# Kernel tuning notes

Hardware: AMD Instinct MI355X
Metric: run time of the kernel (lower is better)

Reference implementation:

```python
import jax, jax.numpy as jnp
import numpy as np

N, L, D = 2, 2048, 96
H, DK, DV = 4, 16, 16
OUT = 96
SPATIAL = H * (3 + 1 + 3)  # points + distance + direction per head
INF = 100000.0
EPS_DIR = 1e-10
EPS_LN = 1e-5


def setup_inputs() -> dict:
    key = jax.random.key(0)
    ks = jax.random.split(key, 10)
    return {
        "x": jax.random.normal(ks[0], (N, L, D), jnp.float32),
        "pos_CA": jax.random.normal(ks[1], (N, L, 3), jnp.float32),
        "pos_CB": jax.random.normal(ks[2], (N, L, 3), jnp.float32),
        "frame": jax.random.normal(ks[3], (N, L, 3, 3), jnp.float32),
        "mask": jnp.ones((N, L), dtype=bool),
        "Wq": jax.random.normal(ks[4], (D, H * DK), jnp.float32) * 0.1,
        "Wk": jax.random.normal(ks[5], (D, H * DK), jnp.float32) * 0.1,
        "Wv": jax.random.normal(ks[6], (D, H * DV), jnp.float32) * 0.1,
        "Wo": jax.random.normal(ks[7], (H * DV + SPATIAL, OUT), jnp.float32) * 0.1,
        "bo": jnp.zeros((OUT,), jnp.float32),
        "gamma": jnp.ones((OUT,), jnp.float32),
        "beta": jnp.zeros((OUT,), jnp.float32),
    }


def reference(x, pos_CA, pos_CB, frame, mask, Wq, Wk, Wv, Wo, bo, gamma, beta):
    n, l, _ = x.shape
    q = (x @ Wq).reshape(n, l, H, DK)
    k = (x @ Wk).reshape(n, l, H, DK)
    v = (x @ Wv).reshape(n, l, H, DV)

    # logits (N, L_q, L_k, H)
    logits = jnp.einsum('blhd,bkhd->blkh', q, k)
    mask_row = mask[:, :, None, None]           # (N, L, 1, 1)
    mask_pair = mask_row & mask[:, None, :, None]
    logits = jnp.where(mask_pair, logits, logits - INF)
    alpha = jax.nn.softmax(logits, axis=2)
    alpha = jnp.where(mask_row, alpha, 0.0)

    feat_node = jnp.einsum('blkh,bkhd->blhd', alpha, v).reshape(n, l, H * DV)

    # rel_pos[b,l,k] = CB[k] - CA[l]
    rel_pos = pos_CB[:, None, :, :] - pos_CA[:, :, None, :]
    atom_pos_bias = jnp.einsum('blkh,blkd->blhd', alpha, rel_pos)  # (N,L,H,3)
    feat_distance = jnp.linalg.norm(atom_pos_bias, axis=-1, keepdims=True)
    feat_points = jnp.einsum('blij,blhj->blhi', frame, atom_pos_bias)
    feat_direction = feat_points / (jnp.linalg.norm(feat_points, axis=-1, keepdims=True) + EPS_DIR)

    feat_spatial = jnp.concatenate([
        feat_points.reshape(n, l, H * 3),
        feat_distance.reshape(n, l, H),
        feat_direction.reshape(n, l, H * 3),
    ], axis=-1)

    feat_all = jnp.concatenate([feat_node, feat_spatial], axis=-1) @ Wo + bo
    feat_all = jnp.where(mask[:, :, None], feat_all, 0.0)

    # output_dim == input_dim -> residual + LayerNorm
    h = x + feat_all
    mu = jnp.mean(h, axis=-1, keepdims=True)
    var = jnp.var(h, axis=-1, keepdims=True)
    return (h - mu) / jnp.sqrt(var + EPS_LN) * gamma + beta
```

## Files before the change

### kernel.cpp

```cpp
#include <hip/hip_runtime.h>
#include <hip/hip_fp16.h>

typedef _Float16 f16;
typedef _Float16 v4h __attribute__((ext_vector_type(4)));
typedef _Float16 v8h __attribute__((ext_vector_type(8)));
typedef short    v4s __attribute__((ext_vector_type(4)));
typedef short    v8s __attribute__((ext_vector_type(8)));
typedef float    v4f __attribute__((ext_vector_type(4)));

#define NB   2
#define LSEQ 2048
#define DIM  96
#define NH   4
#define ROWS 4096
#define NT16 128
#define NT32 64
#define OUTD 96
#define SHIFT 12.0f
#define LOG2E   1.4426950408889634f
#define NSH2    (-17.312340490667562f)

#if __has_builtin(__builtin_amdgcn_mfma_f32_16x16x16f16)
#define MFMA16_F16(A, B, C) __builtin_amdgcn_mfma_f32_16x16x16f16((A), (B), (C), 0, 0, 0)
#else
static __device__ __forceinline__ v4f mfma16_f16_asm(v4h a, v4h b, v4f c) {
    asm volatile("v_mfma_f32_16x16x16_f16 %0, %1, %2, %0"
                 : "+v"(c) : "v"(a), "v"(b));
    return c;
}
#define MFMA16_F16(A, B, C) mfma16_f16_asm((A), (B), (C))
#endif
#define MFMA32_F16(A, B, C) __builtin_amdgcn_mfma_f32_16x16x32_f16((A), (B), (C), 0, 0, 0)
#define MFMA_BF16(A, B, C)  __builtin_amdgcn_mfma_f32_16x16x32_bf16((A), (B), (C), 0, 0, 0)

#if __has_builtin(__builtin_amdgcn_exp2f)
#define EXP2F(x) __builtin_amdgcn_exp2f(x)
#else
#define EXP2F(x) exp2f(x)
#endif

static __device__ __forceinline__ short f2bf(float f) {
    unsigned u = __builtin_bit_cast(unsigned, f);
    u += 0x7FFF + ((u >> 16) & 1);
    return (short)(u >> 16);
}

__global__ __launch_bounds__(256) void proj_kernel(
    const float* __restrict__ x,
    const float* __restrict__ posCB,
    const float* __restrict__ Wq,
    const float* __restrict__ Wk,
    const float* __restrict__ Wv,
    f16*   __restrict__ qf,
    f16*   __restrict__ kf2,
    short* __restrict__ vf,
    short* __restrict__ pf)
{
    const int tid  = threadIdx.x;
    const int wv   = tid >> 6;
    const int lane = tid & 63;
    const int quad = lane >> 4, c16 = lane & 15;
    const int bid  = blockIdx.x;
    const int b    = bid >> 7, t16 = bid & 127;
    const int row0 = bid * 16;

    __shared__ v8h wfragv[12 * 3 * 65];
    f16* wf = (f16*)wfragv;

    v8h xb[3];
    #pragma unroll
    for (int kt = 0; kt < 3; ++kt) {
        const float* xp = x + (size_t)(row0 + c16) * DIM + kt * 32 + quad * 8;
        const v4f x0 = *(const v4f*)xp;
        const v4f x1 = *(const v4f*)(xp + 4);
        v8h h;
        #pragma unroll
        for (int j = 0; j < 4; ++j) { h[j] = (f16)x0[j]; h[4 + j] = (f16)x1[j]; }
        xb[kt] = h;
    }

    {
        const float* Ws[3] = {Wq, Wk, Wv};
        #pragma unroll
        for (int widx = 0; widx < 3; ++widx) {
            const float* W = Ws[widx];
            #pragma unroll
            for (int it = 0; it < 24; ++it) {
                const int flat = it * 256 + tid;
                const int dd = flat >> 6, n = flat & 63;
                const int frag = (widx * 4 + (n >> 4)) * 3 + (dd >> 5);
                wf[frag * 520 + (((dd >> 3) & 3) * 16 + (n & 15)) * 8 + (dd & 7)]
                    = (f16)W[flat];
            }
        }
    }
    __syncthreads();

    #pragma unroll
    for (int u = 0; u < 3; ++u) {
        const int dt = wv * 3 + u;
        v4f acc = {0.f, 0.f, 0.f, 0.f};
        #pragma unroll
        for (int kt = 0; kt < 3; ++kt)
            acc = MFMA32_F16(wfragv[(dt * 3 + kt) * 65 + lane], xb[kt], acc);

        const int widx = dt >> 2, sub = dt & 3;
        const int bh = b * NH + sub;
        if (widx == 0) {
            v4h o;
            #pragma unroll
            for (int r = 0; r < 4; ++r) o[r] = (f16)acc[r];
            *(v4h*)(qf + ((size_t)(bh * NT16 + t16)) * 256 + (c16 + 16 * quad) * 4) = o;
        } else if (widx == 1) {
            v4h o;
            #pragma unroll
            for (int r = 0; r < 4; ++r) o[r] = (f16)acc[r];
            *(v4h*)(kf2 + ((size_t)(bh * NT32 + (t16 >> 1))) * 512
                        + lane * 8 + (t16 & 1) * 4) = o;
        } else {
            short* dst = vf + ((size_t)(bh * NT32 + (t16 >> 1))) * 512
                            + (t16 & 1) * 4 + (c16 & 3);
            #pragma unroll
            for (int r = 0; r < 4; ++r)
                dst[(quad * 4 + r + 16 * (c16 >> 2)) * 8] = f2bf(acc[r]);
        }
    }

    if (bid < NB * NT32) {
        const int b2 = bid >> 6, t2 = bid & 63;
        const int lf = tid & 63, jh = tid >> 6;
        const int n = lf & 15, qS = lf >> 4;
        #pragma unroll
        for (int u2 = 0; u2 < 2; ++u2) {
            const int jSp = jh * 2 + u2;
            const int key = t2 * 32 + (jSp < 4 ? qS * 4 + jSp : 16 + qS * 4 + (jSp & 3));
            float val = 0.f;
            if (n < 3)       val = posCB[((size_t)(b2 * LSEQ + key)) * 3 + n];
            else if (n == 3) val = 1.f;
            pf[((size_t)(b2 * NT32 + t2)) * 512 + lf * 8 + jSp] = f2bf(val);
        }
    }
}

__global__ __launch_bounds__(1024, 1) void attn_epi_kernel(
    const f16*   __restrict__ qf,
    const f16*   __restrict__ kf2,
    const short* __restrict__ vf,
    const short* __restrict__ pf,
    const float* __restrict__ x,
    const float* __restrict__ posCA,
    const float* __restrict__ frame,
    const float* __restrict__ Wo,
    const float* __restrict__ bo,
    const float* __restrict__ gamma,
    const float* __restrict__ beta,
    float*       __restrict__ out)
{
    const int w     = threadIdx.x >> 6;
    const int lane  = threadIdx.x & 63;
    const int head  = w & 3, kq = w >> 2;
    const int b     = blockIdx.x >> 7;
    const int qt    = blockIdx.x & 127;
    const int bh    = b * NH + head;
    const int quad  = lane >> 4, c16 = lane & 15;

    __shared__ float comb[16][64][12];
    __shared__ float feat[16][100];
    __shared__ float aps[16][NH][3];

    const v4h aq = *(const v4h*)(qf + ((size_t)(bh * NT16 + qt)) * 256 + lane * 4);
    const f16*   kb = kf2 + (size_t)bh * NT32 * 512;
    const short* vb = vf  + (size_t)bh * NT32 * 512;
    const short* pb = pf  + (size_t)b  * NT32 * 512;

    v4f O  = {0.f, 0.f, 0.f, 0.f};
    v4f Wa = {0.f, 0.f, 0.f, 0.f};
    const v4f zero = {0.f, 0.f, 0.f, 0.f};
    float psum = 0.f;

    const int t0 = kq * 16;
    v8h bk = *(const v8h*)(kb + (size_t)t0 * 512 + lane * 8);
    v8s bv = *(const v8s*)(vb + (size_t)t0 * 512 + lane * 8);
    v8s bp = *(const v8s*)(pb + (size_t)t0 * 512 + lane * 8);

#define ATTN_STEP(BK, BV, BP) do {                                          \
        const v4h bk0 = __builtin_shufflevector((BK), (BK), 0, 1, 2, 3);    \
        const v4h bk1 = __builtin_shufflevector((BK), (BK), 4, 5, 6, 7);    \
        const v4f S0 = MFMA16_F16(bk0, aq, zero);                           \
        const v4f S1 = MFMA16_F16(bk1, aq, zero);                           \
        v8s ap;                                                             \
        _Pragma("unroll")                                                   \
        for (int r = 0; r < 4; ++r) {                                       \
            const float e0 = EXP2F(fmaf(S0[r], LOG2E, NSH2));               \
            const float e1 = EXP2F(fmaf(S1[r], LOG2E, NSH2));               \
            ap[r]     = f2bf(e0);                                           \
            ap[4 + r] = f2bf(e1);                                           \
            psum += e0 + e1;                                                \
        }                                                                   \
        O  = MFMA_BF16(ap, (BV), O);                                        \
        Wa = MFMA_BF16(ap, (BP), Wa);                                       \
    } while (0)

    #pragma unroll 3
    for (int i = 0; i < 15; ++i) {
        const v8h bkc = bk; const v8s bvc = bv, bpc = bp;
        const size_t off = (size_t)(t0 + i + 1) * 512 + lane * 8;
        bk = *(const v8h*)(kb + off);
        bv = *(const v8s*)(vb + off);
        bp = *(const v8s*)(pb + off);
        ATTN_STEP(bkc, bvc, bpc);
    }
    ATTN_STEP(bk, bv, bp);
#undef ATTN_STEP

    {
        float* cb = &comb[w][lane][0];
        *(v4f*)cb       = O;
        *(v4f*)(cb + 4) = Wa;
        cb[8] = psum;
    }
    __syncthreads();

    const int rowg0 = b * LSEQ + qt * 16;

    if (w < 4) {
        #pragma unroll
        for (int k2 = 1; k2 < 4; ++k2) {
            const float* cb = &comb[k2 * 4 + w][lane][0];
            O    += *(const v4f*)cb;
            Wa   += *(const v4f*)(cb + 4);
            psum += cb[8];
        }
        psum += __shfl_xor(psum, 16);
        psum += __shfl_xor(psum, 32);
        const float inv = 1.f / psum;
        #pragma unroll
        for (int r = 0; r < 4; ++r) {
            const float ir = __shfl(inv, quad * 4 + r);
            feat[quad * 4 + r][w * 16 + c16] = O[r] * ir;
            if (c16 < 3)
                aps[quad * 4 + r][w][c16] = Wa[r] * ir;
        }
    }
    __syncthreads();

    if (lane < 4) {
        const int hh = lane;
        const int grow = rowg0 + w;
        float apb[3];
        #pragma unroll
        for (int j = 0; j < 3; ++j)
            apb[j] = aps[w][hh][j] - posCA[(size_t)grow * 3 + j];
        const float dist = sqrtf(apb[0]*apb[0] + apb[1]*apb[1] + apb[2]*apb[2]);
        float fp[3];
        #pragma unroll
        for (int i = 0; i < 3; ++i) {
            float a = 0.f;
            #pragma unroll
            for (int j = 0; j < 3; ++j)
                a = fmaf(frame[(size_t)grow * 9 + i * 3 + j], apb[j], a);
            fp[i] = a;
        }
        const float fpn  = sqrtf(fp[0]*fp[0] + fp[1]*fp[1] + fp[2]*fp[2]);
        const float rinv = 1.f / (fpn + 1e-10f);
        #pragma unroll
        for (int i = 0; i < 3; ++i) {
            feat[w][64 + hh * 3 + i] = fp[i];
            feat[w][80 + hh * 3 + i] = fp[i] * rinv;
        }
        feat[w][76 + hh] = dist;
    }
    __syncthreads();

    {
        const int grow = rowg0 + w;

        float acc0 = bo[lane];
        #pragma unroll 8
        for (int r2 = 0; r2 < 92; ++r2)
            acc0 = fmaf(feat[w][r2], Wo[r2 * OUTD + lane], acc0);
        const float hv0 = acc0 + x[(size_t)grow * DIM + lane];

        float hv1 = 0.f;
        if (lane < 32) {
            float acc1 = bo[64 + lane];
            #pragma unroll 8
            for (int r2 = 0; r2 < 92; ++r2)
                acc1 = fmaf(feat[w][r2], Wo[r2 * OUTD + 64 + lane], acc1);
            hv1 = acc1 + x[(size_t)grow * DIM + 64 + lane];
        }

        float ls = hv0 + hv1;
        float lq = fmaf(hv0, hv0, hv1 * hv1);
        #pragma unroll
        for (int off = 32; off > 0; off >>= 1) {
            ls += __shfl_xor(ls, off);
            lq += __shfl_xor(lq, off);
        }
        const float mu  = ls * (1.f / OUTD);
        const float var = lq * (1.f / OUTD) - mu * mu;
        const float rs  = rsqrtf(var + 1e-5f);

        out[(size_t)grow * OUTD + lane] = (hv0 - mu) * rs * gamma[lane] + beta[lane];
        if (lane < 32)
            out[(size_t)grow * OUTD + 64 + lane] =
                (hv1 - mu) * rs * gamma[64 + lane] + beta[64 + lane];
    }
}

extern "C" void kernel_launch(void* const* d_in, const int* in_sizes, int n_in,
                              void* d_out, int out_size, void* d_ws, size_t ws_size,
                              hipStream_t stream)
{
    const float* x     = (const float*)d_in[0];
    const float* posCA = (const float*)d_in[1];
    const float* posCB = (const float*)d_in[2];
    const float* frame = (const float*)d_in[3];
    const float* Wq    = (const float*)d_in[5];
    const float* Wk    = (const float*)d_in[6];
    const float* Wv    = (const float*)d_in[7];
    const float* Wo    = (const float*)d_in[8];
    const float* bo    = (const float*)d_in[9];
    const float* gamma = (const float*)d_in[10];
    const float* beta  = (const float*)d_in[11];

    f16*   qf  = (f16*)d_ws;
    f16*   kf2 = qf + (size_t)8 * NT16 * 256;
    short* vf  = (short*)(kf2 + (size_t)8 * NT32 * 512);
    short* pf  = vf + (size_t)8 * NT32 * 512;

    proj_kernel<<<256, 256, 0, stream>>>(x, posCB, Wq, Wk, Wv, qf, kf2, vf, pf);
    attn_epi_kernel<<<NB * NT16, 1024, 0, stream>>>(qf, kf2, vf, pf,
                                                    x, posCA, frame,
                                                    Wo, bo, gamma, beta,
                                                    (float*)d_out);
}
```

Baseline: 104.8 us.

## Split attention and epilogue kernels; each block handles one head over 64 queries

Moves the attention into its own kernel. Each block now serves one head and four 16-query tiles, so every K/V/P fragment loaded is reused across four query tiles instead of one. Key tiles are split across all 16 waves, and partial sums are reduced through shared memory per query tile. The attention result and the point bias go to a workspace buffer that a separate epilogue kernel reads to do the spatial features, the Wo projection and LayerNorm. This adds a third launch, a global round-trip through the workspace, and four sync-heavy reduction rounds per block.

Result: slower. 113.8 us (+8.6%).

```diff
diff --git a/kernel.cpp b/kernel.cpp
--- a/kernel.cpp
+++ b/kernel.cpp
@@ -4,7 +4,6 @@
 typedef _Float16 f16;
 typedef _Float16 v4h __attribute__((ext_vector_type(4)));
 typedef _Float16 v8h __attribute__((ext_vector_type(8)));
-typedef short    v4s __attribute__((ext_vector_type(4)));
 typedef short    v8s __attribute__((ext_vector_type(8)));
 typedef float    v4f __attribute__((ext_vector_type(4)));
 
@@ -142,11 +141,107 @@
     }
 }
 
-__global__ __launch_bounds__(1024, 1) void attn_epi_kernel(
+__global__ __launch_bounds__(1024, 1) void attn_kernel(
     const f16*   __restrict__ qf,
     const f16*   __restrict__ kf2,
     const short* __restrict__ vf,
     const short* __restrict__ pf,
+    float*       __restrict__ med)
+{
+    const int tid  = threadIdx.x;
+    const int w    = tid >> 6;
+    const int lane = tid & 63;
+    const int bid  = blockIdx.x;
+    const int b    = bid >> 7, rem = bid & 127;
+    const int qg   = rem >> 2, head = rem & 3;
+    const int bh   = b * NH + head;
+
+    __shared__ float comb[16][64][12];
+    __shared__ float invl[16];
+
+    const f16*   kb = kf2 + (size_t)bh * NT32 * 512;
+    const short* vb = vf  + (size_t)bh * NT32 * 512;
+    const short* pb = pf  + (size_t)b  * NT32 * 512;
+
+    v4h aq[4];
+    #pragma unroll
+    for (int g = 0; g < 4; ++g)
+        aq[g] = *(const v4h*)(qf + ((size_t)(bh * NT16 + qg * 4 + g)) * 256 + lane * 4);
+
+    const v4f zero = {0.f, 0.f, 0.f, 0.f};
+    v4f O[4], Wa[4];
+    float psum[4] = {0.f, 0.f, 0.f, 0.f};
+    #pragma unroll
+    for (int g = 0; g < 4; ++g) { O[g] = zero; Wa[g] = zero; }
+
+    const int t0 = w * 4;
+    v8h bk = *(const v8h*)(kb + (size_t)t0 * 512 + lane * 8);
+    v8s bv = *(const v8s*)(vb + (size_t)t0 * 512 + lane * 8);
+    v8s bp = *(const v8s*)(pb + (size_t)t0 * 512 + lane * 8);
+
+    #pragma unroll
+    for (int i = 0; i < 4; ++i) {
+        const v8h bkc = bk; const v8s bvc = bv, bpc = bp;
+        if (i < 3) {
+            const size_t off = (size_t)(t0 + i + 1) * 512 + lane * 8;
+            bk = *(const v8h*)(kb + off);
+            bv = *(const v8s*)(vb + off);
+            bp = *(const v8s*)(pb + off);
+        }
+        const v4h bk0 = __builtin_shufflevector(bkc, bkc, 0, 1, 2, 3);
+        const v4h bk1 = __builtin_shufflevector(bkc, bkc, 4, 5, 6, 7);
+        #pragma unroll
+        for (int g = 0; g < 4; ++g) {
+            const v4f S0 = MFMA16_F16(bk0, aq[g], zero);
+            const v4f S1 = MFMA16_F16(bk1, aq[g], zero);
+            v8s ap;
+            #pragma unroll
+            for (int r = 0; r < 4; ++r) {
+                const float e0 = EXP2F(fmaf(S0[r], LOG2E, NSH2));
+                const float e1 = EXP2F(fmaf(S1[r], LOG2E, NSH2));
+                ap[r]     = f2bf(e0);
+                ap[4 + r] = f2bf(e1);
+                psum[g] += e0 + e1;
+            }
+            O[g]  = MFMA_BF16(ap, bvc, O[g]);
+            Wa[g] = MFMA_BF16(ap, bpc, Wa[g]);
+        }
+    }
+
+    const int rowbase = b * LSEQ + qg * 64;
+    for (int g = 0; g < 4; ++g) {
+        float* cb = &comb[w][lane][0];
+        *(v4f*)cb       = O[g];
+        *(v4f*)(cb + 4) = Wa[g];
+        cb[8] = psum[g];
+        __syncthreads();
+
+        float s = 0.f;
+        if (w < 9) {
+            #pragma unroll
+            for (int w2 = 0; w2 < 16; ++w2)
+                s += comb[w2][lane][w];
+            if (w == 8) {
+                s += __shfl_xor(s, 16);
+                s += __shfl_xor(s, 32);
+                if (lane < 16) invl[lane] = 1.f / s;
+            }
+        }
+        __syncthreads();
+
+        if (w < 8) {
+            const int qrow = (lane >> 4) * 4 + (w & 3);
+            const int cc   = lane & 15;
+            const float val = s * invl[qrow];
+            const size_t grow = (size_t)(rowbase + g * 16 + qrow);
+            if (w < 4)        med[grow * 80 + head * 16 + cc] = val;
+            else if (cc < 3)  med[grow * 80 + 64 + head * 3 + cc] = val;
+        }
+    }
+}
+
+__global__ __launch_bounds__(1024) void epi_kernel(
+    const float* __restrict__ med,
     const float* __restrict__ x,
     const float* __restrict__ posCA,
     const float* __restrict__ frame,
@@ -156,101 +251,21 @@
     const float* __restrict__ beta,
     float*       __restrict__ out)
 {
-    const int w     = threadIdx.x >> 6;
-    const int lane  = threadIdx.x & 63;
-    const int head  = w & 3, kq = w >> 2;
-    const int b     = blockIdx.x >> 7;
-    const int qt    = blockIdx.x & 127;
-    const int bh    = b * NH + head;
-    const int quad  = lane >> 4, c16 = lane & 15;
-
-    __shared__ float comb[16][64][12];
+    const int w    = threadIdx.x >> 6;
+    const int lane = threadIdx.x & 63;
+    const int grow = blockIdx.x * 16 + w;
+
     __shared__ float feat[16][100];
-    __shared__ float aps[16][NH][3];
-
-    const v4h aq = *(const v4h*)(qf + ((size_t)(bh * NT16 + qt)) * 256 + lane * 4);
-    const f16*   kb = kf2 + (size_t)bh * NT32 * 512;
-    const short* vb = vf  + (size_t)bh * NT32 * 512;
-    const short* pb = pf  + (size_t)b  * NT32 * 512;
-
-    v4f O  = {0.f, 0.f, 0.f, 0.f};
-    v4f Wa = {0.f, 0.f, 0.f, 0.f};
-    const v4f zero = {0.f, 0.f, 0.f, 0.f};
-    float psum = 0.f;
-
-    const int t0 = kq * 16;
-    v8h bk = *(const v8h*)(kb + (size_t)t0 * 512 + lane * 8);
-    v8s bv = *(const v8s*)(vb + (size_t)t0 * 512 + lane * 8);
-    v8s bp = *(const v8s*)(pb + (size_t)t0 * 512 + lane * 8);
-
-#define ATTN_STEP(BK, BV, BP) do {                                          \
-        const v4h bk0 = __builtin_shufflevector((BK), (BK), 0, 1, 2, 3);    \
-        const v4h bk1 = __builtin_shufflevector((BK), (BK), 4, 5, 6, 7);    \
-        const v4f S0 = MFMA16_F16(bk0, aq, zero);                           \
-        const v4f S1 = MFMA16_F16(bk1, aq, zero);                           \
-        v8s ap;                                                             \
-        _Pragma("unroll")                                                   \
-        for (int r = 0; r < 4; ++r) {                                       \
-            const float e0 = EXP2F(fmaf(S0[r], LOG2E, NSH2));               \
-            const float e1 = EXP2F(fmaf(S1[r], LOG2E, NSH2));               \
-            ap[r]     = f2bf(e0);                                           \
-            ap[4 + r] = f2bf(e1);                                           \
-            psum += e0 + e1;                                                \
-        }                                                                   \
-        O  = MFMA_BF16(ap, (BV), O);                                        \
-        Wa = MFMA_BF16(ap, (BP), Wa);                                       \
-    } while (0)
-
-    #pragma unroll 3
-    for (int i = 0; i < 15; ++i) {
-        const v8h bkc = bk; const v8s bvc = bv, bpc = bp;
-        const size_t off = (size_t)(t0 + i + 1) * 512 + lane * 8;
-        bk = *(const v8h*)(kb + off);
-        bv = *(const v8s*)(vb + off);
-        bp = *(const v8s*)(pb + off);
-        ATTN_STEP(bkc, bvc, bpc);
-    }
-    ATTN_STEP(bk, bv, bp);
-#undef ATTN_STEP
-
-    {
-        float* cb = &comb[w][lane][0];
-        *(v4f*)cb       = O;
-        *(v4f*)(cb + 4) = Wa;
-        cb[8] = psum;
-    }
-    __syncthreads();
-
-    const int rowg0 = b * LSEQ + qt * 16;
-
-    if (w < 4) {
-        #pragma unroll
-        for (int k2 = 1; k2 < 4; ++k2) {
-            const float* cb = &comb[k2 * 4 + w][lane][0];
-            O    += *(const v4f*)cb;
-            Wa   += *(const v4f*)(cb + 4);
-            psum += cb[8];
-        }
-        psum += __shfl_xor(psum, 16);
-        psum += __shfl_xor(psum, 32);
-        const float inv = 1.f / psum;
-        #pragma unroll
-        for (int r = 0; r < 4; ++r) {
-            const float ir = __shfl(inv, quad * 4 + r);
-            feat[quad * 4 + r][w * 16 + c16] = O[r] * ir;
-            if (c16 < 3)
-                aps[quad * 4 + r][w][c16] = Wa[r] * ir;
-        }
-    }
-    __syncthreads();
+
+    feat[w][lane] = med[(size_t)grow * 80 + lane];
 
     if (lane < 4) {
         const int hh = lane;
-        const int grow = rowg0 + w;
         float apb[3];
         #pragma unroll
         for (int j = 0; j < 3; ++j)
-            apb[j] = aps[w][hh][j] - posCA[(size_t)grow * 3 + j];
+            apb[j] = med[(size_t)grow * 80 + 64 + hh * 3 + j]
+                   - posCA[(size_t)grow * 3 + j];
         const float dist = sqrtf(apb[0]*apb[0] + apb[1]*apb[1] + apb[2]*apb[2]);
         float fp[3];
         #pragma unroll
@@ -272,40 +287,36 @@
     }
     __syncthreads();
 
-    {
-        const int grow = rowg0 + w;
-
-        float acc0 = bo[lane];
+    float acc0 = bo[lane];
+    #pragma unroll 8
+    for (int r2 = 0; r2 < 92; ++r2)
+        acc0 = fmaf(feat[w][r2], Wo[r2 * OUTD + lane], acc0);
+    const float hv0 = acc0 + x[(size_t)grow * DIM + lane];
+
+    float hv1 = 0.f;
+    if (lane < 32) {
+        float acc1 = bo[64 + lane];
         #pragma unroll 8
         for (int r2 = 0; r2 < 92; ++r2)
-            acc0 = fmaf(feat[w][r2], Wo[r2 * OUTD + lane], acc0);
-        const float hv0 = acc0 + x[(size_t)grow * DIM + lane];
-
-        float hv1 = 0.f;
-        if (lane < 32) {
-            float acc1 = bo[64 + lane];
-            #pragma unroll 8
-            for (int r2 = 0; r2 < 92; ++r2)
-                acc1 = fmaf(feat[w][r2], Wo[r2 * OUTD + 64 + lane], acc1);
-            hv1 = acc1 + x[(size_t)grow * DIM + 64 + lane];
-        }
-
-        float ls = hv0 + hv1;
-        float lq = fmaf(hv0, hv0, hv1 * hv1);
-        #pragma unroll
-        for (int off = 32; off > 0; off >>= 1) {
-            ls += __shfl_xor(ls, off);
-            lq += __shfl_xor(lq, off);
-        }
-        const float mu  = ls * (1.f / OUTD);
-        const float var = lq * (1.f / OUTD) - mu * mu;
-        const float rs  = rsqrtf(var + 1e-5f);
-
-        out[(size_t)grow * OUTD + lane] = (hv0 - mu) * rs * gamma[lane] + beta[lane];
-        if (lane < 32)
-            out[(size_t)grow * OUTD + 64 + lane] =
-                (hv1 - mu) * rs * gamma[64 + lane] + beta[64 + lane];
-    }
+            acc1 = fmaf(feat[w][r2], Wo[r2 * OUTD + 64 + lane], acc1);
+        hv1 = acc1 + x[(size_t)grow * DIM + 64 + lane];
+    }
+
+    float ls = hv0 + hv1;
+    float lq = fmaf(hv0, hv0, hv1 * hv1);
+    #pragma unroll
+    for (int off = 32; off > 0; off >>= 1) {
+        ls += __shfl_xor(ls, off);
+        lq += __shfl_xor(lq, off);
+    }
+    const float mu  = ls * (1.f / OUTD);
+    const float var = lq * (1.f / OUTD) - mu * mu;
+    const float rs  = rsqrtf(var + 1e-5f);
+
+    out[(size_t)grow * OUTD + lane] = (hv0 - mu) * rs * gamma[lane] + beta[lane];
+    if (lane < 32)
+        out[(size_t)grow * OUTD + 64 + lane] =
+            (hv1 - mu) * rs * gamma[64 + lane] + beta[64 + lane];
 }
 
 extern "C" void kernel_launch(void* const* d_in, const int* in_sizes, int n_in,
@@ -328,10 +339,11 @@
     f16*   kf2 = qf + (size_t)8 * NT16 * 256;
     short* vf  = (short*)(kf2 + (size_t)8 * NT32 * 512);
     short* pf  = vf + (size_t)8 * NT32 * 512;
+    float* med = (float*)(pf + (size_t)NB * NT32 * 512);
 
     proj_kernel<<<256, 256, 0, stream>>>(x, posCB, Wq, Wk, Wv, qf, kf2, vf, pf);
-    attn_epi_kernel<<<NB * NT16, 1024, 0, stream>>>(qf, kf2, vf, pf,
-                                                    x, posCA, frame,
-                                                    Wo, bo, gamma, beta,
-                                                    (float*)d_out);
-}
+    attn_kernel<<<NB * NT16, 1024, 0, stream>>>(qf, kf2, vf, pf, med);
+    epi_kernel<<<ROWS / 16, 1024, 0, stream>>>(med, x, posCA, frame,
+                                               Wo, bo, gamma, beta,
+                                               (float*)d_out);
+}
```

## Compact position fragments, widen projection blocks, double-buffer attention loads

Applied to the files above, without the earlier changes.

The position fragment buffer is compacted to store only the four nonzero columns (xyz plus ones), so each tile takes a quarter of the bytes and only 16 lanes load it while the rest use zeros. The projection kernel moves to 1024 threads so weight staging is spread over more threads, but only four waves do the MFMA work. The attention inner loop is fully unrolled with two-stage prefetch of K/V/P so loads run further ahead of use. This cuts memory traffic and load latency at the cost of higher register pressure.

New measurement: 115.9 us. +10.7%, slower.

```diff
diff --git a/kernel.cpp b/kernel.cpp
--- a/kernel.cpp
+++ b/kernel.cpp
@@ -4,7 +4,6 @@
 typedef _Float16 f16;
 typedef _Float16 v4h __attribute__((ext_vector_type(4)));
 typedef _Float16 v8h __attribute__((ext_vector_type(8)));
-typedef short    v4s __attribute__((ext_vector_type(4)));
 typedef short    v8s __attribute__((ext_vector_type(8)));
 typedef float    v4f __attribute__((ext_vector_type(4)));
 
@@ -45,7 +44,7 @@
     return (short)(u >> 16);
 }
 
-__global__ __launch_bounds__(256) void proj_kernel(
+__global__ __launch_bounds__(1024) void proj_kernel(
     const float* __restrict__ x,
     const float* __restrict__ posCB,
     const float* __restrict__ Wq,
@@ -54,10 +53,10 @@
     f16*   __restrict__ qf,
     f16*   __restrict__ kf2,
     short* __restrict__ vf,
-    short* __restrict__ pf)
+    short* __restrict__ pf2)
 {
     const int tid  = threadIdx.x;
-    const int wv   = tid >> 6;
+    const int w    = tid >> 6;
     const int lane = tid & 63;
     const int quad = lane >> 4, c16 = lane & 15;
     const int bid  = blockIdx.x;
@@ -68,15 +67,17 @@
     f16* wf = (f16*)wfragv;
 
     v8h xb[3];
-    #pragma unroll
-    for (int kt = 0; kt < 3; ++kt) {
-        const float* xp = x + (size_t)(row0 + c16) * DIM + kt * 32 + quad * 8;
-        const v4f x0 = *(const v4f*)xp;
-        const v4f x1 = *(const v4f*)(xp + 4);
-        v8h h;
-        #pragma unroll
-        for (int j = 0; j < 4; ++j) { h[j] = (f16)x0[j]; h[4 + j] = (f16)x1[j]; }
-        xb[kt] = h;
+    if (w < 4) {
+        #pragma unroll
+        for (int kt = 0; kt < 3; ++kt) {
+            const float* xp = x + (size_t)(row0 + c16) * DIM + kt * 32 + quad * 8;
+            const v4f x0 = *(const v4f*)xp;
+            const v4f x1 = *(const v4f*)(xp + 4);
+            v8h h;
+            #pragma unroll
+            for (int j = 0; j < 4; ++j) { h[j] = (f16)x0[j]; h[4 + j] = (f16)x1[j]; }
+            xb[kt] = h;
+        }
     }
 
     {
@@ -85,8 +86,8 @@
         for (int widx = 0; widx < 3; ++widx) {
             const float* W = Ws[widx];
             #pragma unroll
-            for (int it = 0; it < 24; ++it) {
-                const int flat = it * 256 + tid;
+            for (int it = 0; it < 6; ++it) {
+                const int flat = it * 1024 + tid;
                 const int dd = flat >> 6, n = flat & 63;
                 const int frag = (widx * 4 + (n >> 4)) * 3 + (dd >> 5);
                 wf[frag * 520 + (((dd >> 3) & 3) * 16 + (n & 15)) * 8 + (dd & 7)]
@@ -96,49 +97,49 @@
     }
     __syncthreads();
 
-    #pragma unroll
-    for (int u = 0; u < 3; ++u) {
-        const int dt = wv * 3 + u;
-        v4f acc = {0.f, 0.f, 0.f, 0.f};
-        #pragma unroll
-        for (int kt = 0; kt < 3; ++kt)
-            acc = MFMA32_F16(wfragv[(dt * 3 + kt) * 65 + lane], xb[kt], acc);
-
-        const int widx = dt >> 2, sub = dt & 3;
-        const int bh = b * NH + sub;
-        if (widx == 0) {
-            v4h o;
+    if (w < 4) {
+        #pragma unroll
+        for (int u = 0; u < 3; ++u) {
+            const int dt = w * 3 + u;
+            v4f acc = {0.f, 0.f, 0.f, 0.f};
             #pragma unroll
-            for (int r = 0; r < 4; ++r) o[r] = (f16)acc[r];
-            *(v4h*)(qf + ((size_t)(bh * NT16 + t16)) * 256 + (c16 + 16 * quad) * 4) = o;
-        } else if (widx == 1) {
-            v4h o;
-            #pragma unroll
-            for (int r = 0; r < 4; ++r) o[r] = (f16)acc[r];
-            *(v4h*)(kf2 + ((size_t)(bh * NT32 + (t16 >> 1))) * 512
-                        + lane * 8 + (t16 & 1) * 4) = o;
-        } else {
-            short* dst = vf + ((size_t)(bh * NT32 + (t16 >> 1))) * 512
-                            + (t16 & 1) * 4 + (c16 & 3);
-            #pragma unroll
-            for (int r = 0; r < 4; ++r)
-                dst[(quad * 4 + r + 16 * (c16 >> 2)) * 8] = f2bf(acc[r]);
-        }
-    }
-
-    if (bid < NB * NT32) {
+            for (int kt = 0; kt < 3; ++kt)
+                acc = MFMA32_F16(wfragv[(dt * 3 + kt) * 65 + lane], xb[kt], acc);
+
+            const int widx = dt >> 2, sub = dt & 3;
+            const int bh = b * NH + sub;
+            if (widx == 0) {
+                v4h o;
+                #pragma unroll
+                for (int r = 0; r < 4; ++r) o[r] = (f16)acc[r];
+                *(v4h*)(qf + ((size_t)(bh * NT16 + t16)) * 256
+                           + (c16 + 16 * quad) * 4) = o;
+            } else if (widx == 1) {
+                v4h o;
+                #pragma unroll
+                for (int r = 0; r < 4; ++r) o[r] = (f16)acc[r];
+                *(v4h*)(kf2 + ((size_t)(bh * NT32 + (t16 >> 1))) * 512
+                            + lane * 8 + (t16 & 1) * 4) = o;
+            } else {
+                short* dst = vf + ((size_t)(bh * NT32 + (t16 >> 1))) * 512
+                                + (t16 & 1) * 4 + (c16 & 3);
+                #pragma unroll
+                for (int r = 0; r < 4; ++r)
+                    dst[(quad * 4 + r + 16 * (c16 >> 2)) * 8] = f2bf(acc[r]);
+            }
+        }
+    }
+
+    if (bid < NB * NT32 && tid < 128) {
         const int b2 = bid >> 6, t2 = bid & 63;
-        const int lf = tid & 63, jh = tid >> 6;
-        const int n = lf & 15, qS = lf >> 4;
-        #pragma unroll
-        for (int u2 = 0; u2 < 2; ++u2) {
-            const int jSp = jh * 2 + u2;
-            const int key = t2 * 32 + (jSp < 4 ? qS * 4 + jSp : 16 + qS * 4 + (jSp & 3));
-            float val = 0.f;
-            if (n < 3)       val = posCB[((size_t)(b2 * LSEQ + key)) * 3 + n];
-            else if (n == 3) val = 1.f;
-            pf[((size_t)(b2 * NT32 + t2)) * 512 + lf * 8 + jSp] = f2bf(val);
-        }
+        const int q  = tid >> 5;
+        const int c  = (tid >> 3) & 3;
+        const int jj = tid & 7;
+        const int key = t2 * 32 + (jj < 4 ? q * 4 + jj : 16 + q * 4 + (jj - 4));
+        float val;
+        if (c < 3) val = posCB[((size_t)(b2 * LSEQ + key)) * 3 + c];
+        else       val = 1.f;
+        pf2[(((size_t)(b2 * NT32 + t2)) * 4 + q) * 32 + c * 8 + jj] = f2bf(val);
     }
 }
 
@@ -146,7 +147,7 @@
     const f16*   __restrict__ qf,
     const f16*   __restrict__ kf2,
     const short* __restrict__ vf,
-    const short* __restrict__ pf,
+    const short* __restrict__ pf2,
     const float* __restrict__ x,
     const float* __restrict__ posCA,
     const float* __restrict__ frame,
@@ -171,47 +172,68 @@
     const v4h aq = *(const v4h*)(qf + ((size_t)(bh * NT16 + qt)) * 256 + lane * 4);
     const f16*   kb = kf2 + (size_t)bh * NT32 * 512;
     const short* vb = vf  + (size_t)bh * NT32 * 512;
-    const short* pb = pf  + (size_t)b  * NT32 * 512;
+    const short* pb = pf2 + (size_t)b  * NT32 * 128;
 
     v4f O  = {0.f, 0.f, 0.f, 0.f};
     v4f Wa = {0.f, 0.f, 0.f, 0.f};
     const v4f zero = {0.f, 0.f, 0.f, 0.f};
+    const v8s zs = {0, 0, 0, 0, 0, 0, 0, 0};
     float psum = 0.f;
 
     const int t0 = kq * 16;
-    v8h bk = *(const v8h*)(kb + (size_t)t0 * 512 + lane * 8);
-    v8s bv = *(const v8s*)(vb + (size_t)t0 * 512 + lane * 8);
-    v8s bp = *(const v8s*)(pb + (size_t)t0 * 512 + lane * 8);
-
-#define ATTN_STEP(BK, BV, BP) do {                                          \
-        const v4h bk0 = __builtin_shufflevector((BK), (BK), 0, 1, 2, 3);    \
-        const v4h bk1 = __builtin_shufflevector((BK), (BK), 4, 5, 6, 7);    \
-        const v4f S0 = MFMA16_F16(bk0, aq, zero);                           \
-        const v4f S1 = MFMA16_F16(bk1, aq, zero);                           \
-        v8s ap;                                                             \
-        _Pragma("unroll")                                                   \
-        for (int r = 0; r < 4; ++r) {                                       \
-            const float e0 = EXP2F(fmaf(S0[r], LOG2E, NSH2));               \
-            const float e1 = EXP2F(fmaf(S1[r], LOG2E, NSH2));               \
-            ap[r]     = f2bf(e0);                                           \
-            ap[4 + r] = f2bf(e1);                                           \
-            psum += e0 + e1;                                                \
-        }                                                                   \
-        O  = MFMA_BF16(ap, (BV), O);                                        \
-        Wa = MFMA_BF16(ap, (BP), Wa);                                       \
-    } while (0)
-
-    #pragma unroll 3
-    for (int i = 0; i < 15; ++i) {
-        const v8h bkc = bk; const v8s bvc = bv, bpc = bp;
-        const size_t off = (size_t)(t0 + i + 1) * 512 + lane * 8;
-        bk = *(const v8h*)(kb + off);
-        bv = *(const v8s*)(vb + off);
-        bp = *(const v8s*)(pb + off);
-        ATTN_STEP(bkc, bvc, bpc);
-    }
-    ATTN_STEP(bk, bv, bp);
-#undef ATTN_STEP
+
+    v8h bkA, bkB; v8s bvA, bvB, bpA, bpB;
+    {
+        const size_t o0 = (size_t)t0 * 512 + lane * 8;
+        bkA = *(const v8h*)(kb + o0);
+        bvA = *(const v8s*)(vb + o0);
+        bpA = zs;
+        if (c16 < 4) bpA = *(const v8s*)(pb + ((size_t)t0 * 4 + quad) * 32 + c16 * 8);
+        const size_t o1 = (size_t)(t0 + 1) * 512 + lane * 8;
+        bkB = *(const v8h*)(kb + o1);
+        bvB = *(const v8s*)(vb + o1);
+        bpB = zs;
+        if (c16 < 4) bpB = *(const v8s*)(pb + ((size_t)(t0 + 1) * 4 + quad) * 32 + c16 * 8);
+    }
+
+    #pragma unroll
+    for (int i = 0; i < 16; ++i) {
+        const v8h bkc = (i & 1) ? bkB : bkA;
+        const v8s bvc = (i & 1) ? bvB : bvA;
+        const v8s bpc = (i & 1) ? bpB : bpA;
+
+        if (i + 2 < 16) {
+            const int tn = t0 + i + 2;
+            const size_t on = (size_t)tn * 512 + lane * 8;
+            if (i & 1) {
+                bkB = *(const v8h*)(kb + on);
+                bvB = *(const v8s*)(vb + on);
+                if (c16 < 4)
+                    bpB = *(const v8s*)(pb + ((size_t)tn * 4 + quad) * 32 + c16 * 8);
+            } else {
+                bkA = *(const v8h*)(kb + on);
+                bvA = *(const v8s*)(vb + on);
+                if (c16 < 4)
+                    bpA = *(const v8s*)(pb + ((size_t)tn * 4 + quad) * 32 + c16 * 8);
+            }
+        }
+
+        const v4h bk0 = __builtin_shufflevector(bkc, bkc, 0, 1, 2, 3);
+        const v4h bk1 = __builtin_shufflevector(bkc, bkc, 4, 5, 6, 7);
+        const v4f S0 = MFMA16_F16(bk0, aq, zero);
+        const v4f S1 = MFMA16_F16(bk1, aq, zero);
+        v8s ap;
+        #pragma unroll
+        for (int r = 0; r < 4; ++r) {
+            const float e0 = EXP2F(fmaf(S0[r], LOG2E, NSH2));
+            const float e1 = EXP2F(fmaf(S1[r], LOG2E, NSH2));
+            ap[r]     = f2bf(e0);
+            ap[4 + r] = f2bf(e1);
+            psum += e0 + e1;
+        }
+        O  = MFMA_BF16(ap, bvc, O);
+        Wa = MFMA_BF16(ap, bpc, Wa);
+    }
 
     {
         float* cb = &comb[w][lane][0];
@@ -327,11 +349,11 @@
     f16*   qf  = (f16*)d_ws;
     f16*   kf2 = qf + (size_t)8 * NT16 * 256;
     short* vf  = (short*)(kf2 + (size_t)8 * NT32 * 512);
-    short* pf  = vf + (size_t)8 * NT32 * 512;
-
-    proj_kernel<<<256, 256, 0, stream>>>(x, posCB, Wq, Wk, Wv, qf, kf2, vf, pf);
-    attn_epi_kernel<<<NB * NT16, 1024, 0, stream>>>(qf, kf2, vf, pf,
-                                                    x, posCA, frame,
-                                                    Wo, bo, gamma, beta,
-                                                    (float*)d_out);
-}
+    short* pf2 = vf + (size_t)8 * NT32 * 512;
+
+    proj_kernel<<<256, 1024, 0, stream>>>(x, posCB, Wq, Wk, Wv, qf, kf2, vf, pf2);
+    attn_epi_kernel<<<256, 1024, 0, stream>>>(qf, kf2, vf, pf2,
+                                              x, posCA, frame,
+                                              Wo, bo, gamma, beta,
+                                              (float*)d_out);
+}
```
